# Performance work log

Measured on AMD Instinct MI355X. Metric: run time of the kernel, lower is better.

The kernel has to match this reference:

```python
import jax, jax.numpy as jnp
import numpy as np

N = 50000      # nodes
E = 1000000    # edges
D = 64         # in_dim == out_dim
R = 200        # num_rels


def setup_inputs() -> dict:
    key = jax.random.key(0)
    ks = jax.random.split(key, 11)
    return {
        "n_feats": jax.random.normal(ks[0], (N, D), jnp.float32),
        "r_feats": jax.random.normal(ks[1], (R, D), jnp.float32),
        "W_I_w": jax.random.normal(ks[2], (D, D), jnp.float32) * 0.1,
        "W_I_b": jax.random.normal(ks[3], (D,), jnp.float32) * 0.1,
        "W_O_w": jax.random.normal(ks[4], (D, D), jnp.float32) * 0.1,
        "W_O_b": jax.random.normal(ks[5], (D,), jnp.float32) * 0.1,
        "W_R_w": jax.random.normal(ks[6], (D, D), jnp.float32) * 0.1,
        "W_R_b": jax.random.normal(ks[7], (D,), jnp.float32) * 0.1,
        "src": jax.random.randint(ks[8], (E,), 0, N),
        "dst": jax.random.randint(ks[9], (E,), 0, N),
        "etype": jax.random.randint(ks[10], (E,), 0, R),
        "num_rels": R,
    }


def reference(n_feats, r_feats, W_I_w, W_I_b, W_O_w, W_O_b, W_R_w, W_R_b,
              src, dst, etype, num_rels):
    # per-edge composition (comp_fn='sub'): h_src - r[etype]   [E, D]
    comp_h = n_feats[src] - r_feats[etype]
    # conditional linear per edge: W_I for etype < num_rels//2, else W_O
    h_i = comp_h @ W_I_w.T + W_I_b
    h_o = comp_h @ W_O_w.T + W_O_b
    mask = (etype < num_rels // 2)[:, None]
    new_comp_h = jnp.where(mask, h_i, h_o)
    # segment-mean scatter to destination nodes (DGL fn.mean)
    num_nodes = n_feats.shape[0]
    seg_sum = jax.ops.segment_sum(new_comp_h, dst, num_segments=num_nodes)
    deg = jax.ops.segment_sum(jnp.ones((new_comp_h.shape[0],), new_comp_h.dtype),
                              dst, num_segments=num_nodes)
    n_out_feats = seg_sum / jnp.maximum(deg, 1.0)[:, None]
    # dropout in eval mode = identity; no batchnorm, no activation, no self-loop
    r_out_feats = r_feats @ W_R_w.T + W_R_b
    return n_out_feats, r_out_feats
```

## Files before the change

### kernel.cpp

```cpp
#include <hip/hip_runtime.h>


#define DIM 64
#define NPB 8
#define WPAD 68
#define NBUCK 256
#define EPB 4096
#define CAP 8192

__device__ __forceinline__ unsigned int pack_bf16(float2 v) {
    unsigned int a = __float_as_uint(v.x);
    unsigned int b = __float_as_uint(v.y);
    a = (a + 0x7FFFu + ((a >> 16) & 1u)) >> 16;
    b = (b + 0x7FFFu + ((b >> 16) & 1u)) >> 16;
    return (a & 0xFFFFu) | (b << 16);
}

__global__ __launch_bounds__(512) void build_kernel(
    const int* __restrict__ src, const int* __restrict__ dst,
    const int* __restrict__ etype, int* __restrict__ bcur,
    unsigned int* __restrict__ es, int E, int sb,
    const float* __restrict__ n_feats, const float* __restrict__ r_feats,
    unsigned int* __restrict__ nfb, unsigned int* __restrict__ rfb,
    int nN2, int nR2)
{
    __shared__ int cnt[NBUCK];
    __shared__ int loff[NBUCK];
    __shared__ int woff[NBUCK];
    __shared__ int lold[NBUCK];
    __shared__ unsigned int stg[EPB];

    int tid = threadIdx.x;

    if (blockIdx.x >= sb) {
        int i = (blockIdx.x - sb) * 512 + tid;
        if (i < nN2) {
            nfb[i] = pack_bf16(((const float2*)n_feats)[i]);
        } else if (i < nN2 + nR2) {
            int k = i - nN2;
            rfb[k] = pack_bf16(((const float2*)r_feats)[k]);
        }
        return;
    }

    int base = blockIdx.x * EPB;
    int end = min(base + EPB, E);
    int m = end - base;

    if (tid < NBUCK) cnt[tid] = 0;
    __syncthreads();

    unsigned int val[8];
    int bk[8];
    #pragma unroll
    for (int k = 0; k < 8; ++k) {
        int e = base + tid + k * 512;
        if (e < end) {
            unsigned int d = (unsigned)dst[e];
            bk[k] = (int)(d >> 8);
            val[k] = ((d & 255u) << 24) | (((unsigned)src[e]) << 8)
                   | (unsigned)etype[e];
            atomicAdd(&cnt[bk[k]], 1);
        } else {
            bk[k] = -1;
            val[k] = 0u;
        }
    }
    __syncthreads();

    if (tid < NBUCK) loff[tid] = cnt[tid];
    __syncthreads();
    for (int off = 1; off < NBUCK; off <<= 1) {
        int t = 0;
        if (tid < NBUCK && tid >= off) t = loff[tid - off];
        __syncthreads();
        if (tid < NBUCK) loff[tid] += t;
        __syncthreads();
    }
    if (tid < NBUCK) {
        int excl = loff[tid] - cnt[tid];
        woff[tid] = excl;
        lold[tid] = (cnt[tid] > 0) ? atomicAdd(&bcur[tid], cnt[tid]) : 0;
    }
    __syncthreads();

    #pragma unroll
    for (int k = 0; k < 8; ++k) {
        if (bk[k] >= 0) {
            int p = atomicAdd(&woff[bk[k]], 1);
            stg[p] = val[k];
        }
    }
    __syncthreads();

    for (int j = tid; j < m; j += 512) {
        int lo_ = 0, hi_ = NBUCK;
        while (lo_ < hi_) {
            int mid = (lo_ + hi_) >> 1;
            if (loff[mid] > j) hi_ = mid; else lo_ = mid + 1;
        }
        int b = lo_;
        int excl = loff[b] - cnt[b];
        int local = lold[b] + (j - excl);
        if (local < CAP) es[(size_t)b * CAP + local] = stg[j];
    }
}

__global__ __launch_bounds__(512) void bsort_kernel(
    const unsigned int* __restrict__ es, const int* __restrict__ bcur,
    unsigned int* __restrict__ es2, int* __restrict__ rowptr,
    int* __restrict__ deg, int* __restrict__ degI,
    const int* __restrict__ num_rels, int N)
{
    __shared__ unsigned int st[CAP];
    __shared__ int nd[512], nl[512], ncur[512];

    int b = blockIdx.x, tid = threadIdx.x;
    int base = b * CAP;
    int cnt = min(bcur[b], CAP);
    int half = num_rels[0] >> 1;

    nd[tid] = 0;
    for (int j = tid; j < cnt; j += 512) st[j] = es[base + j];
    __syncthreads();

    for (int j = tid; j < cnt; j += 512) {
        unsigned int e = st[j];
        int k = (int)((e >> 24) << 1) | ((int)(e & 0xFFu) >= half ? 1 : 0);
        atomicAdd(&nd[k], 1);
    }
    __syncthreads();

    nl[tid] = nd[tid];
    __syncthreads();
    for (int off = 1; off < 512; off <<= 1) {
        int t = (tid >= off) ? nl[tid - off] : 0;
        __syncthreads();
        nl[tid] += t;
        __syncthreads();
    }
    ncur[tid] = nl[tid] - nd[tid];
    if ((tid & 1) == 0) {
        int v = (b << 8) + (tid >> 1);
        if (v < N) {
            rowptr[v] = base + (nl[tid] - nd[tid]);
            degI[v]   = nd[tid];
            deg[v]    = nd[tid] + nd[tid + 1];
        }
    }
    __syncthreads();

    for (int j = tid; j < cnt; j += 512) {
        unsigned int e = st[j];
        int k = (int)((e >> 24) << 1) | ((int)(e & 0xFFu) >= half ? 1 : 0);
        int p = atomicAdd(&ncur[k], 1);
        es2[base + p] = e;
    }
}

__device__ __forceinline__ void acc8m(const uint4 f, const uint4 r, float w,
                                      float* aT, float* aI) {
    float c;
    c = __uint_as_float(f.x << 16)         - __uint_as_float(r.x << 16);
    aT[0] += c; aI[0] = fmaf(w, c, aI[0]);
    c = __uint_as_float(f.x & 0xFFFF0000u) - __uint_as_float(r.x & 0xFFFF0000u);
    aT[1] += c; aI[1] = fmaf(w, c, aI[1]);
    c = __uint_as_float(f.y << 16)         - __uint_as_float(r.y << 16);
    aT[2] += c; aI[2] = fmaf(w, c, aI[2]);
    c = __uint_as_float(f.y & 0xFFFF0000u) - __uint_as_float(r.y & 0xFFFF0000u);
    aT[3] += c; aI[3] = fmaf(w, c, aI[3]);
    c = __uint_as_float(f.z << 16)         - __uint_as_float(r.z << 16);
    aT[4] += c; aI[4] = fmaf(w, c, aI[4]);
    c = __uint_as_float(f.z & 0xFFFF0000u) - __uint_as_float(r.z & 0xFFFF0000u);
    aT[5] += c; aI[5] = fmaf(w, c, aI[5]);
    c = __uint_as_float(f.w << 16)         - __uint_as_float(r.w << 16);
    aT[6] += c; aI[6] = fmaf(w, c, aI[6]);
    c = __uint_as_float(f.w & 0xFFFF0000u) - __uint_as_float(r.w & 0xFFFF0000u);
    aT[7] += c; aI[7] = fmaf(w, c, aI[7]);
}

__global__ __launch_bounds__(512, 4) void rows_kernel(
    const unsigned int* __restrict__ nfb, const unsigned int* __restrict__ rfb,
    const float* __restrict__ r_feats,
    const int* __restrict__ rowptr, const int* __restrict__ degs,
    const int* __restrict__ degIs, const unsigned int* __restrict__ es2,
    const float* __restrict__ W_I_w, const float* __restrict__ W_I_b,
    const float* __restrict__ W_O_w, const float* __restrict__ W_O_b,
    const float* __restrict__ W_R_w, const float* __restrict__ W_R_b,
    float* __restrict__ n_out, float* __restrict__ r_out, int N, int Rr)
{
    __shared__ float WIp[DIM * WPAD];
    __shared__ float WOp[DIM * WPAD];
    __shared__ float xI[NPB][DIM];
    __shared__ float xO[NPB][DIM];

    const int tid = threadIdx.x;
    for (int i = tid; i < DIM * DIM; i += 512) {
        int j = i >> 6, d = i & 63;
        WIp[j * WPAD + d] = W_I_w[i];
        WOp[j * WPAD + d] = W_O_w[i];
    }
    __syncthreads();

    const int wv = tid >> 6, lane = tid & 63;
    const int e8 = lane >> 3, fl = lane & 7;
    const uint4* nf4 = (const uint4*)nfb;
    const uint4* rf4 = (const uint4*)rfb;

    int row = blockIdx.x * NPB + wv;
    if (row < N) {
        int lo = rowptr[row];
        int dI = degIs[row];
        int dT = degs[row];
        int mid = lo + dI, hi = lo + dT;
        float aI[8] = {0.f, 0.f, 0.f, 0.f, 0.f, 0.f, 0.f, 0.f};
        float aT[8] = {0.f, 0.f, 0.f, 0.f, 0.f, 0.f, 0.f, 0.f};

        int i = lo + e8;
        for (; i + 8 < hi; i += 16) {
            unsigned int ea = es2[i], eb = es2[i + 8];
            uint4 fa = nf4[(size_t)((ea >> 8) & 0xFFFFu) * 8 + fl];
            uint4 ra = rf4[(size_t)(ea & 0xFFu) * 8 + fl];
            uint4 fb = nf4[(size_t)((eb >> 8) & 0xFFFFu) * 8 + fl];
            uint4 rb = rf4[(size_t)(eb & 0xFFu) * 8 + fl];
            float wa = (i < mid) ? 1.0f : 0.0f;
            float wb = (i + 8 < mid) ? 1.0f : 0.0f;
            acc8m(fa, ra, wa, aT, aI);
            acc8m(fb, rb, wb, aT, aI);
        }
        for (; i < hi; i += 8) {
            unsigned int ea = es2[i];
            uint4 fa = nf4[(size_t)((ea >> 8) & 0xFFFFu) * 8 + fl];
            uint4 ra = rf4[(size_t)(ea & 0xFFu) * 8 + fl];
            float wa = (i < mid) ? 1.0f : 0.0f;
            acc8m(fa, ra, wa, aT, aI);
        }

        #pragma unroll
        for (int d = 8; d < 64; d <<= 1) {
            #pragma unroll
            for (int k = 0; k < 8; ++k) {
                aT[k] += __shfl_xor(aT[k], d, 64);
                aI[k] += __shfl_xor(aI[k], d, 64);
            }
        }
        if (e8 == 0) {
            #pragma unroll
            for (int k = 0; k < 8; ++k) {
                xI[wv][fl * 8 + k] = aI[k];
                xO[wv][fl * 8 + k] = aT[k] - aI[k];
            }
        }

        float sum = (float)dI * W_I_b[lane] + (float)(dT - dI) * W_O_b[lane];
        #pragma unroll
        for (int d4 = 0; d4 < DIM; d4 += 4) {
            float4 wi = *(const float4*)&WIp[lane * WPAD + d4];
            float4 wo = *(const float4*)&WOp[lane * WPAD + d4];
            float4 xi = *(const float4*)&xI[wv][d4];
            float4 xo = *(const float4*)&xO[wv][d4];
            sum += wi.x*xi.x + wi.y*xi.y + wi.z*xi.z + wi.w*xi.w
                 + wo.x*xo.x + wo.y*xo.y + wo.z*xo.z + wo.w*xo.w;
        }
        __builtin_nontemporal_store(sum / (float)(dT > 1 ? dT : 1),
                                    &n_out[(size_t)row * DIM + lane]);
    } else if (row < N + Rr) {
        int r = row - N;
        const float4* wr4 = (const float4*)W_R_w;
        const float4* rr4 = (const float4*)r_feats;
        float sum = W_R_b[lane];
        #pragma unroll
        for (int d4 = 0; d4 < 16; ++d4) {
            float4 w = wr4[(size_t)lane * 16 + d4];
            float4 x = rr4[(size_t)r * 16 + d4];
            sum += w.x*x.x + w.y*x.y + w.z*x.z + w.w*x.w;
        }
        __builtin_nontemporal_store(sum, &r_out[(size_t)r * DIM + lane]);
    }
}

extern "C" void kernel_launch(void* const* d_in, const int* in_sizes, int n_in,
                              void* d_out, int out_size, void* d_ws, size_t ws_size,
                              hipStream_t stream) {
    const float* n_feats  = (const float*)d_in[0];
    const float* r_feats  = (const float*)d_in[1];
    const float* W_I_w    = (const float*)d_in[2];
    const float* W_I_b    = (const float*)d_in[3];
    const float* W_O_w    = (const float*)d_in[4];
    const float* W_O_b    = (const float*)d_in[5];
    const float* W_R_w    = (const float*)d_in[6];
    const float* W_R_b    = (const float*)d_in[7];
    const int*   src      = (const int*)d_in[8];
    const int*   dst      = (const int*)d_in[9];
    const int*   etype    = (const int*)d_in[10];
    const int*   num_rels = (const int*)d_in[11];

    const int N  = in_sizes[0] / DIM;
    const int Rr = in_sizes[1] / DIM;
    const int E  = in_sizes[8];

    unsigned int* es   = (unsigned int*)d_ws;
    unsigned int* es2  = es + (size_t)NBUCK * CAP;
    unsigned int* nfb  = es2 + (size_t)NBUCK * CAP;
    unsigned int* rfb  = nfb + (size_t)N * (DIM / 2);
    int* bcur   = (int*)(rfb + (size_t)Rr * (DIM / 2));
    int* rowptr = bcur + NBUCK;
    int* deg    = rowptr + N;
    int* degI   = deg + N;

    float* n_out = (float*)d_out;
    float* r_out = n_out + (size_t)N * DIM;

    hipMemsetAsync(bcur, 0, NBUCK * sizeof(int), stream);

    int nN2 = N * (DIM / 2), nR2 = Rr * (DIM / 2);
    int sb = (E + EPB - 1) / EPB;
    int cvtB = (nN2 + nR2 + 511) / 512;
    build_kernel<<<sb + cvtB, 512, 0, stream>>>(
        src, dst, etype, bcur, es, E, sb,
        n_feats, r_feats, nfb, rfb, nN2, nR2);

    int nbUsed = (N + 255) >> 8;
    bsort_kernel<<<nbUsed, 512, 0, stream>>>(
        es, bcur, es2, rowptr, deg, degI, num_rels, N);

    int rowsBlocks = (N + Rr + NPB - 1) / NPB;
    rows_kernel<<<rowsBlocks, 512, 0, stream>>>(
        nfb, rfb, r_feats, rowptr, deg, degI, es2,
        W_I_w, W_I_b, W_O_w, W_O_b, W_R_w, W_R_b,
        n_out, r_out, N, Rr);
}
```

Measured before the change: 186.8 us.

## Gather 8 lanes per node and apply linear via bf16 MFMA per 64-node tile

Each node's gather now uses 8 threads (each owning 8 features) walking edges sequentially, instead of a whole wavefront with shuffle reductions, so one 512-thread block handles 64 nodes. The per-node aggregated I/O sums are packed to bf16 in shared memory and multiplied by bf16 W_I/W_O using 16x16x32 MFMA instructions, replacing the scalar fp32 dot products. This removes cross-lane reduction and per-row weight-matrix work, but adds bf16 rounding of the aggregates and weights, and leaves load imbalance between nodes of different degree within each 8-lane group.

```diff
diff --git a/kernel.cpp b/kernel.cpp
--- a/kernel.cpp
+++ b/kernel.cpp
@@ -2,11 +2,12 @@
 
 
 #define DIM 64
-#define NPB 8
-#define WPAD 68
 #define NBUCK 256
 #define EPB 4096
 #define CAP 8192
+
+typedef __attribute__((ext_vector_type(8))) short bfrag8_t;
+typedef __attribute__((ext_vector_type(4))) float facc4_t;
 
 __device__ __forceinline__ unsigned int pack_bf16(float2 v) {
     unsigned int a = __float_as_uint(v.x);
@@ -179,7 +180,7 @@
     aT[7] += c; aI[7] = fmaf(w, c, aI[7]);
 }
 
-__global__ __launch_bounds__(512, 4) void rows_kernel(
+__global__ __launch_bounds__(512) void rows_kernel(
     const unsigned int* __restrict__ nfb, const unsigned int* __restrict__ rfb,
     const float* __restrict__ r_feats,
     const int* __restrict__ rowptr, const int* __restrict__ degs,
@@ -187,95 +188,118 @@
     const float* __restrict__ W_I_w, const float* __restrict__ W_I_b,
     const float* __restrict__ W_O_w, const float* __restrict__ W_O_b,
     const float* __restrict__ W_R_w, const float* __restrict__ W_R_b,
-    float* __restrict__ n_out, float* __restrict__ r_out, int N, int Rr)
+    float* __restrict__ n_out, float* __restrict__ r_out,
+    int N, int Rr, int nodeBlocks)
 {
-    __shared__ float WIp[DIM * WPAD];
-    __shared__ float WOp[DIM * WPAD];
-    __shared__ float xI[NPB][DIM];
-    __shared__ float xO[NPB][DIM];
-
-    const int tid = threadIdx.x;
-    for (int i = tid; i < DIM * DIM; i += 512) {
-        int j = i >> 6, d = i & 63;
-        WIp[j * WPAD + d] = W_I_w[i];
-        WOp[j * WPAD + d] = W_O_w[i];
-    }
-    __syncthreads();
-
-    const int wv = tid >> 6, lane = tid & 63;
-    const int e8 = lane >> 3, fl = lane & 7;
+    __shared__ unsigned int accL[64][68];
+    __shared__ unsigned int wtL[64][68];
+
+    int tid = threadIdx.x;
+
+    if (blockIdx.x >= nodeBlocks) {
+        int wv = tid >> 6, lane = tid & 63;
+        int r = (blockIdx.x - nodeBlocks) * 8 + wv;
+        if (r < Rr) {
+            const float4* wr4 = (const float4*)W_R_w;
+            const float4* rr4 = (const float4*)r_feats;
+            float sum = W_R_b[lane];
+            #pragma unroll
+            for (int d4 = 0; d4 < 16; ++d4) {
+                float4 w = wr4[(size_t)lane * 16 + d4];
+                float4 x = rr4[(size_t)r * 16 + d4];
+                sum += w.x*x.x + w.y*x.y + w.z*x.z + w.w*x.w;
+            }
+            __builtin_nontemporal_store(sum, &r_out[(size_t)r * DIM + lane]);
+        }
+        return;
+    }
+
+    for (int x = tid; x < 2048; x += 512) {
+        int j = x >> 5, p = x & 31;
+        float2 wi = ((const float2*)W_I_w)[j * 32 + p];
+        float2 wo = ((const float2*)W_O_w)[j * 32 + p];
+        wtL[j][p]      = pack_bf16(make_float2(wi.x, wi.y));
+        wtL[j][32 + p] = pack_bf16(make_float2(wo.x, wo.y));
+    }
+
+    int g  = tid >> 3;
+    int fl = tid & 7;
+    int row = blockIdx.x * 64 + g;
+
+    float aT[8] = {0.f,0.f,0.f,0.f,0.f,0.f,0.f,0.f};
+    float aI[8] = {0.f,0.f,0.f,0.f,0.f,0.f,0.f,0.f};
     const uint4* nf4 = (const uint4*)nfb;
     const uint4* rf4 = (const uint4*)rfb;
 
-    int row = blockIdx.x * NPB + wv;
     if (row < N) {
         int lo = rowptr[row];
-        int dI = degIs[row];
-        int dT = degs[row];
-        int mid = lo + dI, hi = lo + dT;
-        float aI[8] = {0.f, 0.f, 0.f, 0.f, 0.f, 0.f, 0.f, 0.f};
-        float aT[8] = {0.f, 0.f, 0.f, 0.f, 0.f, 0.f, 0.f, 0.f};
-
-        int i = lo + e8;
-        for (; i + 8 < hi; i += 16) {
-            unsigned int ea = es2[i], eb = es2[i + 8];
-            uint4 fa = nf4[(size_t)((ea >> 8) & 0xFFFFu) * 8 + fl];
-            uint4 ra = rf4[(size_t)(ea & 0xFFu) * 8 + fl];
-            uint4 fb = nf4[(size_t)((eb >> 8) & 0xFFFFu) * 8 + fl];
-            uint4 rb = rf4[(size_t)(eb & 0xFFu) * 8 + fl];
-            float wa = (i < mid) ? 1.0f : 0.0f;
-            float wb = (i + 8 < mid) ? 1.0f : 0.0f;
-            acc8m(fa, ra, wa, aT, aI);
-            acc8m(fb, rb, wb, aT, aI);
-        }
-        for (; i < hi; i += 8) {
-            unsigned int ea = es2[i];
-            uint4 fa = nf4[(size_t)((ea >> 8) & 0xFFFFu) * 8 + fl];
-            uint4 ra = rf4[(size_t)(ea & 0xFFu) * 8 + fl];
-            float wa = (i < mid) ? 1.0f : 0.0f;
-            acc8m(fa, ra, wa, aT, aI);
-        }
-
+        int mid = lo + degIs[row];
+        int hi = lo + degs[row];
+        int i = lo;
+        for (; i + 3 < hi; i += 4) {
+            unsigned int e0 = es2[i],     e1 = es2[i + 1];
+            unsigned int e2 = es2[i + 2], e3 = es2[i + 3];
+            uint4 f0 = nf4[(size_t)((e0 >> 8) & 0xFFFFu) * 8 + fl];
+            uint4 r0 = rf4[(size_t)(e0 & 0xFFu) * 8 + fl];
+            uint4 f1 = nf4[(size_t)((e1 >> 8) & 0xFFFFu) * 8 + fl];
+            uint4 r1 = rf4[(size_t)(e1 & 0xFFu) * 8 + fl];
+            uint4 f2 = nf4[(size_t)((e2 >> 8) & 0xFFFFu) * 8 + fl];
+            uint4 r2 = rf4[(size_t)(e2 & 0xFFu) * 8 + fl];
+            uint4 f3 = nf4[(size_t)((e3 >> 8) & 0xFFFFu) * 8 + fl];
+            uint4 r3 = rf4[(size_t)(e3 & 0xFFu) * 8 + fl];
+            acc8m(f0, r0, (i     < mid) ? 1.0f : 0.0f, aT, aI);
+            acc8m(f1, r1, (i + 1 < mid) ? 1.0f : 0.0f, aT, aI);
+            acc8m(f2, r2, (i + 2 < mid) ? 1.0f : 0.0f, aT, aI);
+            acc8m(f3, r3, (i + 3 < mid) ? 1.0f : 0.0f, aT, aI);
+        }
+        for (; i < hi; ++i) {
+            unsigned int e0 = es2[i];
+            uint4 f0 = nf4[(size_t)((e0 >> 8) & 0xFFFFu) * 8 + fl];
+            uint4 r0 = rf4[(size_t)(e0 & 0xFFu) * 8 + fl];
+            acc8m(f0, r0, (i < mid) ? 1.0f : 0.0f, aT, aI);
+        }
+    }
+
+    uint4 pI, pO;
+    pI.x = pack_bf16(make_float2(aI[0], aI[1]));
+    pI.y = pack_bf16(make_float2(aI[2], aI[3]));
+    pI.z = pack_bf16(make_float2(aI[4], aI[5]));
+    pI.w = pack_bf16(make_float2(aI[6], aI[7]));
+    pO.x = pack_bf16(make_float2(aT[0] - aI[0], aT[1] - aI[1]));
+    pO.y = pack_bf16(make_float2(aT[2] - aI[2], aT[3] - aI[3]));
+    pO.z = pack_bf16(make_float2(aT[4] - aI[4], aT[5] - aI[5]));
+    pO.w = pack_bf16(make_float2(aT[6] - aI[6], aT[7] - aI[7]));
+    *(uint4*)&accL[g][fl * 4]      = pI;
+    *(uint4*)&accL[g][32 + fl * 4] = pO;
+    __syncthreads();
+
+    int wv = tid >> 6, lane = tid & 63;
+    int lr = lane & 15, kb = lane >> 4;
+    int mt = wv & 3;
+    #pragma unroll
+    for (int t = 0; t < 2; ++t) {
+        int nt = (wv >> 2) * 2 + t;
+        facc4_t c = {0.f, 0.f, 0.f, 0.f};
         #pragma unroll
-        for (int d = 8; d < 64; d <<= 1) {
-            #pragma unroll
-            for (int k = 0; k < 8; ++k) {
-                aT[k] += __shfl_xor(aT[k], d, 64);
-                aI[k] += __shfl_xor(aI[k], d, 64);
+        for (int kt = 0; kt < 4; ++kt) {
+            bfrag8_t a = *(const bfrag8_t*)&accL[mt * 16 + lr][kt * 16 + kb * 4];
+            bfrag8_t b = *(const bfrag8_t*)&wtL[nt * 16 + lr][kt * 16 + kb * 4];
+            c = __builtin_amdgcn_mfma_f32_16x16x32_bf16(a, b, c, 0, 0, 0);
+        }
+        int col = nt * 16 + lr;
+        float bIc = W_I_b[col], bOc = W_O_b[col];
+        #pragma unroll
+        for (int rI = 0; rI < 4; ++rI) {
+            int lrow = mt * 16 + kb * 4 + rI;
+            int v = blockIdx.x * 64 + lrow;
+            if (v < N) {
+                float dI = (float)degIs[v];
+                float dT = (float)degs[v];
+                float s = c[rI] + dI * bIc + (dT - dI) * bOc;
+                float den = dT > 1.f ? dT : 1.f;
+                __builtin_nontemporal_store(s / den, &n_out[(size_t)v * DIM + col]);
             }
         }
-        if (e8 == 0) {
-            #pragma unroll
-            for (int k = 0; k < 8; ++k) {
-                xI[wv][fl * 8 + k] = aI[k];
-                xO[wv][fl * 8 + k] = aT[k] - aI[k];
-            }
-        }
-
-        float sum = (float)dI * W_I_b[lane] + (float)(dT - dI) * W_O_b[lane];
-        #pragma unroll
-        for (int d4 = 0; d4 < DIM; d4 += 4) {
-            float4 wi = *(const float4*)&WIp[lane * WPAD + d4];
-            float4 wo = *(const float4*)&WOp[lane * WPAD + d4];
-            float4 xi = *(const float4*)&xI[wv][d4];
-            float4 xo = *(const float4*)&xO[wv][d4];
-            sum += wi.x*xi.x + wi.y*xi.y + wi.z*xi.z + wi.w*xi.w
-                 + wo.x*xo.x + wo.y*xo.y + wo.z*xo.z + wo.w*xo.w;
-        }
-        __builtin_nontemporal_store(sum / (float)(dT > 1 ? dT : 1),
-                                    &n_out[(size_t)row * DIM + lane]);
-    } else if (row < N + Rr) {
-        int r = row - N;
-        const float4* wr4 = (const float4*)W_R_w;
-        const float4* rr4 = (const float4*)r_feats;
-        float sum = W_R_b[lane];
-        #pragma unroll
-        for (int d4 = 0; d4 < 16; ++d4) {
-            float4 w = wr4[(size_t)lane * 16 + d4];
-            float4 x = rr4[(size_t)r * 16 + d4];
-            sum += w.x*x.x + w.y*x.y + w.z*x.z + w.w*x.w;
-        }
-        __builtin_nontemporal_store(sum, &r_out[(size_t)r * DIM + lane]);
     }
 }
 
@@ -324,9 +348,10 @@
     bsort_kernel<<<nbUsed, 512, 0, stream>>>(
         es, bcur, es2, rowptr, deg, degI, num_rels, N);
 
-    int rowsBlocks = (N + Rr + NPB - 1) / NPB;
-    rows_kernel<<<rowsBlocks, 512, 0, stream>>>(
+    int nodeBlocks = (N + 63) / 64;
+    int relBlocks  = (Rr + 7) / 8;
+    rows_kernel<<<nodeBlocks + relBlocks, 512, 0, stream>>>(
         nfb, rfb, r_feats, rowptr, deg, degI, es2,
         W_I_w, W_I_b, W_O_w, W_O_b, W_R_w, W_R_b,
-        n_out, r_out, N, Rr);
-}
+        n_out, r_out, N, Rr, nodeBlocks);
+}
```

New measurement: 154.4 us. -17.4%, faster.
